# Performance work log

Hardware: AMD Instinct MI355X
Metric: run time of the kernel (lower is better)

Reference implementation:

```python
import jax, jax.numpy as jnp
import numpy as np

B, S, D, H = 8, 8192, 256, 256


def setup_inputs() -> dict:
    key = jax.random.key(0)
    ks = jax.random.split(key, 5)
    scale = 1.0 / np.sqrt(D)  # mimic nn.Linear init scale
    return {
        "x": jax.random.normal(ks[0], (B, S, D), dtype=jnp.float32),
        "h0": jnp.zeros((B, 1, H), dtype=jnp.float32),
        "w_h_w": jax.random.normal(ks[1], (H, D), dtype=jnp.float32) * scale,
        "w_h_b": jax.random.normal(ks[2], (H,), dtype=jnp.float32) * scale,
        "w_z_w": jax.random.normal(ks[3], (H, D), dtype=jnp.float32) * scale,
        "w_z_b": jax.random.normal(ks[4], (H,), dtype=jnp.float32) * scale,
    }


def reference(x, h0, w_h_w, w_h_b, w_z_w, w_z_b):
    # Projections over the whole sequence (same math as per-step Linear calls)
    z = jax.nn.sigmoid(jnp.einsum('bsd,hd->bsh', x, w_z_w) + w_z_b)  # [B,S,H]
    h_tilde = jnp.einsum('bsd,hd->bsh', x, w_h_w) + w_h_b            # [B,S,H]

    def step(h_prev, zh):
        z_t, ht_t = zh  # each [B,H]
        h_t = (1.0 - z_t) * h_prev + z_t * ht_t
        return h_t, h_t

    # scan over time axis; carry is [B,H]
    _, hs = jax.lax.scan(step, h0[:, 0],
                         (jnp.swapaxes(z, 0, 1), jnp.swapaxes(h_tilde, 0, 1)))
    return jnp.swapaxes(hs, 0, 1)  # [B,S,H]
```

## Files before the change

### kernel.cpp

```cpp
#include <hip/hip_runtime.h>
#include <math.h>


constexpr int B_ = 8;
constexpr int S_ = 8192;
constexpr int D_ = 256;
constexpr int H_ = 256;
constexpr int M_ = B_ * S_;
constexpr int CHUNKS = 128;
constexpr int CLEN = S_ / CHUNKS;

typedef __attribute__((ext_vector_type(8))) short bf16x8;
typedef __attribute__((ext_vector_type(4))) float f32x4;

__device__ __forceinline__ ushort f2bf(float f) {
  union { float f; uint u; } v; v.f = f;
  const uint r = v.u + 0x7FFFu + ((v.u >> 16) & 1u);
  return (ushort)(r >> 16);
}

__global__ __launch_bounds__(256) void gemm_zh(
    const float* __restrict__ x,
    const float* __restrict__ whw, const float* __restrict__ whb,
    const float* __restrict__ wzw, const float* __restrict__ wzb,
    uint* __restrict__ ab)
{
  __shared__ ushort xs[128][72];
  __shared__ ushort wzs[64][72];
  __shared__ ushort whs[64][72];

  const int tid = threadIdx.x;
  const int g    = blockIdx.x;
  const int xcd  = g & 7;
  const int loc  = g >> 3;
  const int nt   = loc & 3;
  const int panel = (loc >> 2) * 8 + xcd;
  const int m0 = panel * 128;
  const int n0 = nt * 64;

  const int lane = tid & 63;
  const int w  = tid >> 6;
  const int mb = (w & 1) * 64;
  const int nb = (w >> 1) * 32;
  const int q  = lane >> 4;
  const int cn = lane & 15;

  f32x4 accz[4][2] = {};
  f32x4 acch[4][2] = {};

  for (int k0 = 0; k0 < D_; k0 += 64) {
    __syncthreads();
#pragma unroll
    for (int f = 0; f < 8; f++) {
      const int idx = tid + 256 * f;
      const int row = idx >> 4, seg = idx & 15;
      float4 v = *(const float4*)(x + (size_t)(m0 + row) * D_ + k0 + seg * 4);
      *(ushort4*)&xs[row][seg * 4] =
          make_ushort4(f2bf(v.x), f2bf(v.y), f2bf(v.z), f2bf(v.w));
    }
#pragma unroll
    for (int f = 0; f < 4; f++) {
      const int idx = tid + 256 * f;
      const int row = idx >> 4, seg = idx & 15;
      float4 vz = *(const float4*)(wzw + (size_t)(n0 + row) * D_ + k0 + seg * 4);
      float4 vh = *(const float4*)(whw + (size_t)(n0 + row) * D_ + k0 + seg * 4);
      *(ushort4*)&wzs[row][seg * 4] =
          make_ushort4(f2bf(vz.x), f2bf(vz.y), f2bf(vz.z), f2bf(vz.w));
      *(ushort4*)&whs[row][seg * 4] =
          make_ushort4(f2bf(vh.x), f2bf(vh.y), f2bf(vh.z), f2bf(vh.w));
    }
    __syncthreads();
#pragma unroll
    for (int ks = 0; ks < 2; ks++) {
      const int kk = ks * 32 + q * 8;
      bf16x8 af[4], bz[2], bh[2];
#pragma unroll
      for (int i = 0; i < 4; i++)
        af[i] = *(const bf16x8*)&xs[mb + i * 16 + cn][kk];
#pragma unroll
      for (int j = 0; j < 2; j++) {
        bz[j] = *(const bf16x8*)&wzs[nb + j * 16 + cn][kk];
        bh[j] = *(const bf16x8*)&whs[nb + j * 16 + cn][kk];
      }
#pragma unroll
      for (int i = 0; i < 4; i++)
#pragma unroll
        for (int j = 0; j < 2; j++) {
          accz[i][j] = __builtin_amdgcn_mfma_f32_16x16x32_bf16(af[i], bz[j], accz[i][j], 0, 0, 0);
          acch[i][j] = __builtin_amdgcn_mfma_f32_16x16x32_bf16(af[i], bh[j], acch[i][j], 0, 0, 0);
        }
    }
  }

#pragma unroll
  for (int j = 0; j < 2; j++) {
    const int ch = n0 + nb + j * 16 + cn;
    const float zb = wzb[ch], hb = whb[ch];
#pragma unroll
    for (int i = 0; i < 4; i++) {
#pragma unroll
      for (int r = 0; r < 4; r++) {
        const int row = m0 + mb + i * 16 + q * 4 + r;
        const float zpre = accz[i][j][r] + zb;
        const float hpre = acch[i][j][r] + hb;
        const float zs = 1.0f / (1.0f + __expf(-zpre));
        const ushort ua = f2bf(1.0f - zs);
        const ushort ub = f2bf(zs * hpre);
        ab[(size_t)row * H_ + ch] = ((uint)ub << 16) | (uint)ua;
      }
    }
  }
}

__global__ __launch_bounds__(256) void scan_phaseA(
    const uint* __restrict__ ab,
    float* __restrict__ P_out, float* __restrict__ Q_out)
{
  const int half = threadIdx.x >> 7;
  const int lt   = threadIdx.x & 127;
  const int c = blockIdx.x * 2 + half;
  const int b = blockIdx.y;
  const int ch = lt * 2;
  size_t base = ((size_t)b * S_ + (size_t)c * CLEN) * H_ + ch;
  float P0 = 1.f, P1 = 1.f, Q0 = 0.f, Q1 = 0.f;
  for (int t0 = 0; t0 < CLEN; t0 += 8) {
    uint2 v[8];
#pragma unroll
    for (int j = 0; j < 8; j++)
      v[j] = *(const uint2*)(ab + base + (size_t)(t0 + j) * H_);
#pragma unroll
    for (int j = 0; j < 8; j++) {
      const float a0 = __uint_as_float(v[j].x << 16);
      const float b0 = __uint_as_float(v[j].x & 0xFFFF0000u);
      const float a1 = __uint_as_float(v[j].y << 16);
      const float b1 = __uint_as_float(v[j].y & 0xFFFF0000u);
      Q0 = fmaf(a0, Q0, b0); P0 *= a0;
      Q1 = fmaf(a1, Q1, b1); P1 *= a1;
    }
  }
  const size_t idx = ((size_t)b * CHUNKS + c) * H_ + ch;
  *(float2*)(P_out + idx) = make_float2(P0, P1);
  *(float2*)(Q_out + idx) = make_float2(Q0, Q1);
}

__global__ __launch_bounds__(256) void scan_phaseB(
    const float* __restrict__ h0in, const float* __restrict__ P,
    const float* __restrict__ Q, float* __restrict__ hstate)
{
  const int b = blockIdx.x;
  const int h = threadIdx.x;
  float hc = h0in[(size_t)b * H_ + h];
  for (int c = 0; c < CHUNKS; c++) {
    const size_t idx = ((size_t)b * CHUNKS + c) * H_ + h;
    hstate[idx] = hc;
    hc = fmaf(P[idx], hc, Q[idx]);
  }
}

__global__ __launch_bounds__(256) void scan_phaseC(
    const uint* __restrict__ ab, const float* __restrict__ hstate,
    float* __restrict__ out)
{
  const int half = threadIdx.x >> 7;
  const int lt   = threadIdx.x & 127;
  const int c = blockIdx.x * 2 + half;
  const int b = blockIdx.y;
  const int ch = lt * 2;
  size_t base = ((size_t)b * S_ + (size_t)c * CLEN) * H_ + ch;
  float2 h = *(const float2*)(hstate + ((size_t)b * CHUNKS + c) * H_ + ch);
  for (int t0 = 0; t0 < CLEN; t0 += 8) {
    uint2 v[8];
#pragma unroll
    for (int j = 0; j < 8; j++)
      v[j] = *(const uint2*)(ab + base + (size_t)(t0 + j) * H_);
#pragma unroll
    for (int j = 0; j < 8; j++) {
      const float a0 = __uint_as_float(v[j].x << 16);
      const float b0 = __uint_as_float(v[j].x & 0xFFFF0000u);
      const float a1 = __uint_as_float(v[j].y << 16);
      const float b1 = __uint_as_float(v[j].y & 0xFFFF0000u);
      h.x = fmaf(a0, h.x, b0);
      h.y = fmaf(a1, h.y, b1);
      *(float2*)(out + base + (size_t)(t0 + j) * H_) = h;
    }
  }
}

extern "C" void kernel_launch(void* const* d_in, const int* in_sizes, int n_in,
                              void* d_out, int out_size, void* d_ws, size_t ws_size,
                              hipStream_t stream) {
  const float* x   = (const float*)d_in[0];
  const float* h0  = (const float*)d_in[1];
  const float* whw = (const float*)d_in[2];
  const float* whb = (const float*)d_in[3];
  const float* wzw = (const float*)d_in[4];
  const float* wzb = (const float*)d_in[5];
  float* out = (float*)d_out;

  uint*  ab     = (uint*)d_ws;
  float* chunkP = (float*)(ab + (size_t)M_ * H_);
  float* chunkQ = chunkP + (size_t)B_ * CHUNKS * H_;
  float* hstate = chunkQ + (size_t)B_ * CHUNKS * H_;

  gemm_zh<<<(M_ / 128) * 4, 256, 0, stream>>>(x, whw, whb, wzw, wzb, ab);
  scan_phaseA<<<dim3(CHUNKS / 2, B_), 256, 0, stream>>>(ab, chunkP, chunkQ);
  scan_phaseB<<<B_, 256, 0, stream>>>(h0, chunkP, chunkQ, hstate);
  scan_phaseC<<<dim3(CHUNKS / 2, B_), 256, 0, stream>>>(ab, hstate, out);
}
```

Before: 197.8 us.

## Cheapen bf16 packing and sigmoid, remap scan threads to one channel each

Replaces the round-to-nearest-even bf16 conversion with a round-half-up add followed by a single byte-permute that packs two values. Computes the sigmoid terms with a hardware reciprocal, so 1-z becomes e*rcp. Changes the scan phases A and C to one channel per thread with twice as many blocks, and batches the phase B loads eight chunks at a time to expose memory parallelism. The rounding mode changes slightly and the accesses per thread narrow from 8 bytes to 4.

```diff
diff --git a/kernel.cpp b/kernel.cpp
--- a/kernel.cpp
+++ b/kernel.cpp
@@ -13,10 +13,10 @@
 typedef __attribute__((ext_vector_type(8))) short bf16x8;
 typedef __attribute__((ext_vector_type(4))) float f32x4;
 
-__device__ __forceinline__ ushort f2bf(float f) {
-  union { float f; uint u; } v; v.f = f;
-  const uint r = v.u + 0x7FFFu + ((v.u >> 16) & 1u);
-  return (ushort)(r >> 16);
+__device__ __forceinline__ uint pack2bf(float f0, float f1) {
+  const uint u0 = __float_as_uint(f0) + 0x8000u;
+  const uint u1 = __float_as_uint(f1) + 0x8000u;
+  return __builtin_amdgcn_perm(u1, u0, 0x07060302u);
 }
 
 __global__ __launch_bounds__(256) void gemm_zh(
@@ -55,8 +55,8 @@
       const int idx = tid + 256 * f;
       const int row = idx >> 4, seg = idx & 15;
       float4 v = *(const float4*)(x + (size_t)(m0 + row) * D_ + k0 + seg * 4);
-      *(ushort4*)&xs[row][seg * 4] =
-          make_ushort4(f2bf(v.x), f2bf(v.y), f2bf(v.z), f2bf(v.w));
+      *(uint2*)&xs[row][seg * 4] =
+          make_uint2(pack2bf(v.x, v.y), pack2bf(v.z, v.w));
     }
 #pragma unroll
     for (int f = 0; f < 4; f++) {
@@ -64,10 +64,10 @@
       const int row = idx >> 4, seg = idx & 15;
       float4 vz = *(const float4*)(wzw + (size_t)(n0 + row) * D_ + k0 + seg * 4);
       float4 vh = *(const float4*)(whw + (size_t)(n0 + row) * D_ + k0 + seg * 4);
-      *(ushort4*)&wzs[row][seg * 4] =
-          make_ushort4(f2bf(vz.x), f2bf(vz.y), f2bf(vz.z), f2bf(vz.w));
-      *(ushort4*)&whs[row][seg * 4] =
-          make_ushort4(f2bf(vh.x), f2bf(vh.y), f2bf(vh.z), f2bf(vh.w));
+      *(uint2*)&wzs[row][seg * 4] =
+          make_uint2(pack2bf(vz.x, vz.y), pack2bf(vz.z, vz.w));
+      *(uint2*)&whs[row][seg * 4] =
+          make_uint2(pack2bf(vh.x, vh.y), pack2bf(vh.z, vh.w));
     }
     __syncthreads();
 #pragma unroll
@@ -103,10 +103,9 @@
         const int row = m0 + mb + i * 16 + q * 4 + r;
         const float zpre = accz[i][j][r] + zb;
         const float hpre = acch[i][j][r] + hb;
-        const float zs = 1.0f / (1.0f + __expf(-zpre));
-        const ushort ua = f2bf(1.0f - zs);
-        const ushort ub = f2bf(zs * hpre);
-        ab[(size_t)row * H_ + ch] = ((uint)ub << 16) | (uint)ua;
+        const float e = __expf(-zpre);
+        const float rcp = __builtin_amdgcn_rcpf(1.0f + e);
+        ab[(size_t)row * H_ + ch] = pack2bf(e * rcp, hpre * rcp);
       }
     }
   }
@@ -116,31 +115,27 @@
     const uint* __restrict__ ab,
     float* __restrict__ P_out, float* __restrict__ Q_out)
 {
-  const int half = threadIdx.x >> 7;
-  const int lt   = threadIdx.x & 127;
-  const int c = blockIdx.x * 2 + half;
+  const int c = blockIdx.x;
   const int b = blockIdx.y;
-  const int ch = lt * 2;
+  const int ch = threadIdx.x;
   size_t base = ((size_t)b * S_ + (size_t)c * CLEN) * H_ + ch;
-  float P0 = 1.f, P1 = 1.f, Q0 = 0.f, Q1 = 0.f;
+  float P = 1.f, Q = 0.f;
   for (int t0 = 0; t0 < CLEN; t0 += 8) {
-    uint2 v[8];
+    uint v[8];
 #pragma unroll
     for (int j = 0; j < 8; j++)
-      v[j] = *(const uint2*)(ab + base + (size_t)(t0 + j) * H_);
-#pragma unroll
-    for (int j = 0; j < 8; j++) {
-      const float a0 = __uint_as_float(v[j].x << 16);
-      const float b0 = __uint_as_float(v[j].x & 0xFFFF0000u);
-      const float a1 = __uint_as_float(v[j].y << 16);
-      const float b1 = __uint_as_float(v[j].y & 0xFFFF0000u);
-      Q0 = fmaf(a0, Q0, b0); P0 *= a0;
-      Q1 = fmaf(a1, Q1, b1); P1 *= a1;
+      v[j] = ab[base + (size_t)(t0 + j) * H_];
+#pragma unroll
+    for (int j = 0; j < 8; j++) {
+      const float a = __uint_as_float(v[j] << 16);
+      const float bb = __uint_as_float(v[j] & 0xFFFF0000u);
+      Q = fmaf(a, Q, bb);
+      P *= a;
     }
   }
   const size_t idx = ((size_t)b * CHUNKS + c) * H_ + ch;
-  *(float2*)(P_out + idx) = make_float2(P0, P1);
-  *(float2*)(Q_out + idx) = make_float2(Q0, Q1);
+  P_out[idx] = P;
+  Q_out[idx] = Q;
 }
 
 __global__ __launch_bounds__(256) void scan_phaseB(
@@ -149,11 +144,20 @@
 {
   const int b = blockIdx.x;
   const int h = threadIdx.x;
+  const size_t base = (size_t)b * CHUNKS * H_ + h;
   float hc = h0in[(size_t)b * H_ + h];
-  for (int c = 0; c < CHUNKS; c++) {
-    const size_t idx = ((size_t)b * CHUNKS + c) * H_ + h;
-    hstate[idx] = hc;
-    hc = fmaf(P[idx], hc, Q[idx]);
+  for (int c0 = 0; c0 < CHUNKS; c0 += 8) {
+    float p[8], q[8];
+#pragma unroll
+    for (int j = 0; j < 8; j++) {
+      p[j] = P[base + (size_t)(c0 + j) * H_];
+      q[j] = Q[base + (size_t)(c0 + j) * H_];
+    }
+#pragma unroll
+    for (int j = 0; j < 8; j++) {
+      hstate[base + (size_t)(c0 + j) * H_] = hc;
+      hc = fmaf(p[j], hc, q[j]);
+    }
   }
 }
 
@@ -161,27 +165,22 @@
     const uint* __restrict__ ab, const float* __restrict__ hstate,
     float* __restrict__ out)
 {
-  const int half = threadIdx.x >> 7;
-  const int lt   = threadIdx.x & 127;
-  const int c = blockIdx.x * 2 + half;
+  const int c = blockIdx.x;
   const int b = blockIdx.y;
-  const int ch = lt * 2;
+  const int ch = threadIdx.x;
   size_t base = ((size_t)b * S_ + (size_t)c * CLEN) * H_ + ch;
-  float2 h = *(const float2*)(hstate + ((size_t)b * CHUNKS + c) * H_ + ch);
+  float hc = hstate[((size_t)b * CHUNKS + c) * H_ + ch];
   for (int t0 = 0; t0 < CLEN; t0 += 8) {
-    uint2 v[8];
+    uint v[8];
 #pragma unroll
     for (int j = 0; j < 8; j++)
-      v[j] = *(const uint2*)(ab + base + (size_t)(t0 + j) * H_);
-#pragma unroll
-    for (int j = 0; j < 8; j++) {
-      const float a0 = __uint_as_float(v[j].x << 16);
-      const float b0 = __uint_as_float(v[j].x & 0xFFFF0000u);
-      const float a1 = __uint_as_float(v[j].y << 16);
-      const float b1 = __uint_as_float(v[j].y & 0xFFFF0000u);
-      h.x = fmaf(a0, h.x, b0);
-      h.y = fmaf(a1, h.y, b1);
-      *(float2*)(out + base + (size_t)(t0 + j) * H_) = h;
+      v[j] = ab[base + (size_t)(t0 + j) * H_];
+#pragma unroll
+    for (int j = 0; j < 8; j++) {
+      const float a = __uint_as_float(v[j] << 16);
+      const float bb = __uint_as_float(v[j] & 0xFFFF0000u);
+      hc = fmaf(a, hc, bb);
+      out[base + (size_t)(t0 + j) * H_] = hc;
     }
   }
 }
@@ -203,7 +202,7 @@
   float* hstate = chunkQ + (size_t)B_ * CHUNKS * H_;
 
   gemm_zh<<<(M_ / 128) * 4, 256, 0, stream>>>(x, whw, whb, wzw, wzb, ab);
-  scan_phaseA<<<dim3(CHUNKS / 2, B_), 256, 0, stream>>>(ab, chunkP, chunkQ);
+  scan_phaseA<<<dim3(CHUNKS, B_), 256, 0, stream>>>(ab, chunkP, chunkQ);
   scan_phaseB<<<B_, 256, 0, stream>>>(h0, chunkP, chunkQ, hstate);
-  scan_phaseC<<<dim3(CHUNKS / 2, B_), 256, 0, stream>>>(ab, hstate, out);
-}
+  scan_phaseC<<<dim3(CHUNKS, B_), 256, 0, stream>>>(ab, hstate, out);
+}
```

Measured after the change: 191.1 us. 3.4% less time.
